# Optimization experiments

Measured on AMD Instinct MI355X. Metric: run time of the kernel, lower is better.

## Reference

```python
import jax, jax.numpy as jnp
import numpy as np

ALPHA = 0.1        # axis_aligned_projection threshold
NEG_INF = -1e30    # large negative used for masking (softmax-equivalent to -inf)


def axis_aligned_projection(x, alpha=ALPHA):
    x_abs = jnp.abs(x)
    max_vals = jnp.max(x_abs, axis=-1, keepdims=True)
    axis_weights = jnp.where(x_abs >= alpha * max_vals, x_abs, 0.0)
    return axis_weights * jnp.sign(x)


def setup_inputs() -> dict:
    key = jax.random.key(0)
    kq, kk, kv = jax.random.split(key, 3)
    B, L, H, E = 4, 2048, 8, 64
    S, D = L, E
    queries = jax.random.normal(kq, (B, L, H, E), dtype=jnp.float32)
    keys = jax.random.normal(kk, (B, S, H, E), dtype=jnp.float32)
    values = jax.random.normal(kv, (B, S, H, D), dtype=jnp.float32)
    # TriangularCausalMask: True strictly above the diagonal -> masked out
    causal = jnp.triu(jnp.ones((L, S), dtype=jnp.bool_), k=1)
    attn_mask = jnp.broadcast_to(causal[None, None], (B, 1, L, S))
    return {"queries": queries, "keys": keys, "values": values, "attn_mask": attn_mask}


def reference(queries, keys, values, attn_mask):
    B, L, H, E = queries.shape
    scale = 1.0 / jnp.sqrt(jnp.float32(E))
    q = axis_aligned_projection(queries)
    k = axis_aligned_projection(keys)
    # [B,H,L,S] dense scores (the module materializes the full matrix)
    scores = jnp.einsum('blhe,bshe->bhls', q, k)
    scores = jnp.where(attn_mask, NEG_INF, scores)
    A = jax.nn.softmax(scale * scores, axis=-1)  # dropout is identity in eval mode
    V = jnp.einsum('bhls,bshd->blhd', A, values)
    return V
```

## Files before the change

### kernel.cpp

```cpp
#include <hip/hip_runtime.h>
#include <hip/hip_bf16.h>
#include <stdint.h>

#define B_ 4
#define L_ 2048
#define H_ 8
#define E_ 64
#define ALPHA 0.1f
#define LOG2E 1.44269504088896f
#define QSCALE (0.125f * LOG2E)


typedef float f32x4 __attribute__((ext_vector_type(4)));
typedef short bf16x8 __attribute__((ext_vector_type(8)));
typedef short bf16x4 __attribute__((ext_vector_type(4)));
typedef uint32_t u32;
typedef unsigned short u16;
typedef u32 u32x2 __attribute__((ext_vector_type(2)));

__device__ __forceinline__ u16 f2bf(float f) {
    u32 x = __builtin_bit_cast(u32, f);
    u32 r = x + 0x7fffu + ((x >> 16) & 1u);
    return (u16)(r >> 16);
}

__device__ __forceinline__ u32 pk2bf(float a, float b) {
    u32 ua = __builtin_bit_cast(u32, a) + 0x8000u;
    u32 ub = __builtin_bit_cast(u32, b) + 0x8000u;
    return (ua >> 16) | (ub & 0xffff0000u);
}

__device__ __forceinline__ f32x4 mfma16x16x16bf16(bf16x4 a, bf16x4 b, f32x4 c) {
#if __has_builtin(__builtin_amdgcn_mfma_f32_16x16x16bf16_1k)
    return __builtin_amdgcn_mfma_f32_16x16x16bf16_1k(a, b, c, 0, 0, 0);
#elif __has_builtin(__builtin_amdgcn_mfma_f32_16x16x16_bf16)
    return __builtin_amdgcn_mfma_f32_16x16x16_bf16(a, b, c, 0, 0, 0);
#else
    f32x4 d;
    asm volatile("v_mfma_f32_16x16x16_bf16 %0, %1, %2, %3"
                 : "=v"(d) : "v"(a), "v"(b), "v"(c));
    return d;
#endif
}

__device__ __forceinline__ void dma16(const u16* g, u16* l) {
    __builtin_amdgcn_global_load_lds(
        (const __attribute__((address_space(1))) void*)g,
        (__attribute__((address_space(3))) void*)l, 16, 0, 0);
}

__global__ __launch_bounds__(256) void prep_kernel(const float* __restrict__ qin,
                                                   const float* __restrict__ kin,
                                                   const float* __restrict__ vin,
                                                   u16* __restrict__ qp,
                                                   u16* __restrict__ kp,
                                                   u16* __restrict__ vt) {
    __shared__ u16 tile[64][66];
    if (blockIdx.x < 4096) {
        const int RG = (B_ * L_ * H_) / 8;
        int wave = threadIdx.x >> 6, lane = threadIdx.x & 63;
        int g = blockIdx.x * 4 + wave;
        const float* src;
        u16* dst;
        int gr;
        float sc;
        bool isq;
        if (g < RG) { src = qin; dst = qp; gr = g; sc = QSCALE; isq = true; }
        else        { src = kin; dst = kp; gr = g - RG; sc = 1.0f; isq = false; }

        int rig = lane >> 3;
        int j = lane & 7;
        int c = j * 4;
        int row = gr * 8 + rig;

        const float* rp = src + (size_t)row * 64;
        float4 v0 = *(const float4*)(rp + c);
        float4 v1 = *(const float4*)(rp + c + 32);
        float f[8] = {v0.x, v0.y, v0.z, v0.w, v1.x, v1.y, v1.z, v1.w};

        float mx = 0.f;
#pragma unroll
        for (int i = 0; i < 8; ++i) mx = fmaxf(mx, fabsf(f[i]));
#pragma unroll
        for (int m = 1; m < 8; m <<= 1) mx = fmaxf(mx, __shfl_xor(mx, m));
        float thr = ALPHA * mx;

        u16 o[8];
#pragma unroll
        for (int i = 0; i < 8; ++i)
            o[i] = (fabsf(f[i]) >= thr) ? f2bf(f[i] * sc) : (u16)0;

        int b = row >> 14;
        int l = (row >> 3) & (L_ - 1);
        int h = row & 7;
        int e0, e1;
        if (isq) {
            e0 = c;
            e1 = c + 32;
        } else {
            int l7 = l & 7;
            e0 = (((j >> 1) ^ l7) << 3) + ((j & 1) << 2);
            e1 = ((((j >> 1) + 4) ^ l7) << 3) + ((j & 1) << 2);
        }
        u16* orow = dst + ((size_t)(b * H_ + h) * L_ + l) * 64;
        uint2 p0 = {(u32)o[0] | ((u32)o[1] << 16), (u32)o[2] | ((u32)o[3] << 16)};
        uint2 p1 = {(u32)o[4] | ((u32)o[5] << 16), (u32)o[6] | ((u32)o[7] << 16)};
        *(uint2*)(orow + e0) = p0;
        *(uint2*)(orow + e1) = p1;
    } else {
        int bx = blockIdx.x - 4096;
        int bh = bx >> 5, sblk = bx & 31;
        int b = bh >> 3, h = bh & 7;
        int t = threadIdx.x;
        int s0 = sblk * 64;

#pragma unroll
        for (int p = 0; p < 2; ++p) {
            int sl = p * 32 + (t >> 3);
            int c = (t & 7) * 4;
            const float* rp = vin + (((size_t)(b * L_ + s0 + sl)) * H_ + h) * 64;
            float4 a = *(const float4*)(rp + c);
            float4 bb = *(const float4*)(rp + c + 32);
            u32* d0 = (u32*)&tile[sl][c];
            d0[0] = (u32)f2bf(a.x) | ((u32)f2bf(a.y) << 16);
            d0[1] = (u32)f2bf(a.z) | ((u32)f2bf(a.w) << 16);
            u32* d1 = (u32*)&tile[sl][c + 32];
            d1[0] = (u32)f2bf(bb.x) | ((u32)f2bf(bb.y) << 16);
            d1[1] = (u32)f2bf(bb.z) | ((u32)f2bf(bb.w) << 16);
        }
        __syncthreads();
#pragma unroll
        for (int p = 0; p < 2; ++p) {
            int d = p * 32 + (t >> 3);
            int c16 = t & 7;
            int sc2 = c16 * 8;
            u16 o[8];
#pragma unroll
            for (int i = 0; i < 8; ++i) o[i] = tile[sc2 + i][d];
            u32 w0 = (u32)o[0] | ((u32)o[1] << 16);
            u32 w1 = (u32)o[2] | ((u32)o[3] << 16);
            u32 w2 = (u32)o[4] | ((u32)o[5] << 16);
            u32 w3 = (u32)o[6] | ((u32)o[7] << 16);
            uint4 val;
            if (d & 1) { val.x = w2; val.y = w3; val.z = w0; val.w = w1; }
            else       { val.x = w0; val.y = w1; val.z = w2; val.w = w3; }
            int pc = c16 ^ ((d >> 1) & 7);
            *(uint4*)(vt + ((size_t)(bh * 32 + sblk) * 64 + d) * 64 + pc * 8) = val;
        }
    }
}

__global__ __launch_bounds__(256, 4) void flash_kernel(const u16* __restrict__ Qp,
                                                       const u16* __restrict__ Kp,
                                                       const u16* __restrict__ Vt,
                                                       float* __restrict__ out) {
    __shared__ u16 kbuf[2][64 * 64];
    __shared__ u16 vbuf[2][64 * 64];
    int t = threadIdx.x;
    int wave = t >> 6, lane = t & 63;
    int bh = blockIdx.x & 31;
    int r5 = blockIdx.x >> 5;
    int g = r5 & 7, kr = r5 >> 3;
    int qq = (kr == 0) ? (31 - g) : (kr == 1) ? (16 + g) : (kr == 2) ? (15 - g) : g;
    int lo = lane & 15, quad = lane >> 4;
    int lo7 = lo & 7;
    int q0 = qq * 64 + wave * 16;
    int b = bh >> 3, h = bh & 7;

    int kc0 = (quad ^ lo7) << 3;
    int kc1 = ((quad + 4) ^ lo7) << 3;

    u32x2 onespk = {0x3F803F80u, 0x3F803F80u};
    bf16x4 vONES = __builtin_bit_cast(bf16x4, onespk);

    const u16* kg0 = Kp + (size_t)bh * L_ * 64 + wave * 512 + lane * 8;
    const u16* vg0 = Vt + (size_t)bh * 32 * 64 * 64 + wave * 512 + lane * 8;

    auto stage = [&](int kt, int buf) {
        const u16* kg = kg0 + (size_t)kt * 4096;
        const u16* vg = vg0 + (size_t)kt * 4096;
        u16* kl = kbuf[buf] + wave * 512;
        u16* vl = vbuf[buf] + wave * 512;
        dma16(kg, kl);
        dma16(kg + 2048, kl + 2048);
        dma16(vg, vl);
        dma16(vg + 2048, vl + 2048);
    };

    const u16* qbase = Qp + ((size_t)bh * L_ + q0 + lo) * 64 + quad * 8;
    bf16x8 aQ0 = *(const bf16x8*)(qbase);
    bf16x8 aQ1 = *(const bf16x8*)(qbase + 32);
    asm volatile("" :: "v"(aQ0), "v"(aQ1));

    f32x4 o[4];
#pragma unroll
    for (int ni = 0; ni < 4; ++ni) o[ni] = (f32x4){0.f, 0.f, 0.f, 0.f};
    f32x4 oL = (f32x4){0.f, 0.f, 0.f, 0.f};

    auto tile_proc = [&](const u16* ks, const u16* vs) {
        bf16x8 k0[4], k1[4];
#pragma unroll
        for (int sub = 0; sub < 4; ++sub) {
            const u16* krow = ks + ((sub * 16 + lo) << 6);
            k0[sub] = *(const bf16x8*)(krow + kc0);
            k1[sub] = *(const bf16x8*)(krow + kc1);
        }
        bf16x4 vf[4][4];
#pragma unroll
        for (int sub = 0; sub < 4; ++sub) {
            int vsw = ((sub * 4 + quad) ^ lo) << 2;
#pragma unroll
            for (int ni = 0; ni < 4; ++ni)
                vf[sub][ni] = *(const bf16x4*)(vs + ((ni * 16 + lo) << 6) + vsw);
        }
        f32x4 S[4];
#pragma unroll
        for (int sub = 0; sub < 4; ++sub) {
            f32x4 acc = {0.f, 0.f, 0.f, 0.f};
            acc = __builtin_amdgcn_mfma_f32_16x16x32_bf16(k0[sub], aQ0, acc, 0, 0, 0);
            S[sub] = __builtin_amdgcn_mfma_f32_16x16x32_bf16(k1[sub], aQ1, acc, 0, 0, 0);
        }
        bf16x4 aP[4];
#pragma unroll
        for (int sub = 0; sub < 4; ++sub) {
            float P0 = __builtin_amdgcn_exp2f(S[sub][0]);
            float P1 = __builtin_amdgcn_exp2f(S[sub][1]);
            float P2 = __builtin_amdgcn_exp2f(S[sub][2]);
            float P3 = __builtin_amdgcn_exp2f(S[sub][3]);
            u32x2 pk = {pk2bf(P0, P1), pk2bf(P2, P3)};
            aP[sub] = __builtin_bit_cast(bf16x4, pk);
        }
#pragma unroll
        for (int sub = 0; sub < 4; ++sub) {
#pragma unroll
            for (int ni = 0; ni < 4; ++ni)
                o[ni] = mfma16x16x16bf16(aP[sub], vf[sub][ni], o[ni]);
            oL = mfma16x16x16bf16(aP[sub], vONES, oL);
        }
    };

    auto frag_proc = [&](const u16* ks, const u16* vs, int sub, bool diag) {
        const u16* krow = ks + ((sub * 16 + lo) << 6);
        bf16x8 k0 = *(const bf16x8*)(krow + kc0);
        bf16x8 k1 = *(const bf16x8*)(krow + kc1);
        f32x4 S = {0.f, 0.f, 0.f, 0.f};
        S = __builtin_amdgcn_mfma_f32_16x16x32_bf16(k0, aQ0, S, 0, 0, 0);
        S = __builtin_amdgcn_mfma_f32_16x16x32_bf16(k1, aQ1, S, 0, 0, 0);

        int vsw = ((sub * 4 + quad) ^ lo) << 2;
        bf16x4 vf[4];
#pragma unroll
        for (int ni = 0; ni < 4; ++ni)
            vf[ni] = *(const bf16x4*)(vs + ((ni * 16 + lo) << 6) + vsw);

        float P[4];
#pragma unroll
        for (int r = 0; r < 4; ++r) {
            float e = __builtin_amdgcn_exp2f(S[r]);
            P[r] = (diag && (quad * 4 + r > lo)) ? 0.f : e;
        }
        u32x2 pk = {pk2bf(P[0], P[1]), pk2bf(P[2], P[3])};
        bf16x4 aP = __builtin_bit_cast(bf16x4, pk);
#pragma unroll
        for (int ni = 0; ni < 4; ++ni)
            o[ni] = mfma16x16x16bf16(aP, vf[ni], o[ni]);
        oL = mfma16x16x16bf16(aP, vONES, oL);
    };

    stage(0, 0);
    __syncthreads();

    for (int kt = 0; kt < qq; ++kt) {
        int cur = kt & 1;
        stage(kt + 1, cur ^ 1);
        tile_proc(kbuf[cur], vbuf[cur]);
        __syncthreads();
    }

    {
        int cur = qq & 1;
        const u16* ks = kbuf[cur];
        const u16* vs = vbuf[cur];
        for (int sub = 0; sub < wave; ++sub) frag_proc(ks, vs, sub, false);
        frag_proc(ks, vs, wave, true);
    }

#pragma unroll
    for (int r = 0; r < 4; ++r) {
        float inv = 1.0f / oL[r];
        int q = q0 + quad * 4 + r;
        float* ob = out + (((size_t)(b * L_ + q)) * H_ + h) * 64 + lo;
        ob[0]  = o[0][r] * inv;
        ob[16] = o[1][r] * inv;
        ob[32] = o[2][r] * inv;
        ob[48] = o[3][r] * inv;
    }
}

extern "C" void kernel_launch(void* const* d_in, const int* in_sizes, int n_in,
                              void* d_out, int out_size, void* d_ws, size_t ws_size,
                              hipStream_t stream) {
    const float* q = (const float*)d_in[0];
    const float* k = (const float*)d_in[1];
    const float* v = (const float*)d_in[2];
    float* out = (float*)d_out;

    const size_t QSZ = (size_t)B_ * H_ * L_ * 64;
    u16* qp = (u16*)d_ws;
    u16* kp = qp + QSZ;
    u16* vt = kp + QSZ;

    prep_kernel<<<5120, 256, 0, stream>>>(q, k, v, qp, kp, vt);
    flash_kernel<<<1024, 256, 0, stream>>>(qp, kp, vt, out);
}
```

Measured before the change: 162.9 us.

## Compute softmax row sums with VALU adds and deepen K/V prefetch pipeline

Replaces the extra MFMA against a ones vector for the softmax denominator with per-lane FP32 adds of the exponentials, followed by a cross-lane shuffle reduction at the end. It also changes the double-buffered load loop to prefetch two tiles ahead, using explicit vmcnt waits and raw barriers instead of __syncthreads. This is meant to cut one MFMA per sub-tile and overlap global-to-LDS DMA more fully with compute. The row sum is now taken from FP32 values rather than the bf16-rounded P, which changes numerics slightly, and the hand-placed waitcnt counts must match the number of outstanding DMAs.

After: 158.0 us, median of 2. -3.0%, faster.

```diff
diff --git a/kernel.cpp b/kernel.cpp
--- a/kernel.cpp
+++ b/kernel.cpp
@@ -170,9 +170,6 @@
     int kc0 = (quad ^ lo7) << 3;
     int kc1 = ((quad + 4) ^ lo7) << 3;
 
-    u32x2 onespk = {0x3F803F80u, 0x3F803F80u};
-    bf16x4 vONES = __builtin_bit_cast(bf16x4, onespk);
-
     const u16* kg0 = Kp + (size_t)bh * L_ * 64 + wave * 512 + lane * 8;
     const u16* vg0 = Vt + (size_t)bh * 32 * 64 * 64 + wave * 512 + lane * 8;
 
@@ -195,7 +192,7 @@
     f32x4 o[4];
 #pragma unroll
     for (int ni = 0; ni < 4; ++ni) o[ni] = (f32x4){0.f, 0.f, 0.f, 0.f};
-    f32x4 oL = (f32x4){0.f, 0.f, 0.f, 0.f};
+    float ls = 0.f;
 
     auto tile_proc = [&](const u16* ks, const u16* vs) {
         bf16x8 k0[4], k1[4];
@@ -227,16 +224,15 @@
             float P1 = __builtin_amdgcn_exp2f(S[sub][1]);
             float P2 = __builtin_amdgcn_exp2f(S[sub][2]);
             float P3 = __builtin_amdgcn_exp2f(S[sub][3]);
+            ls += (P0 + P1) + (P2 + P3);
             u32x2 pk = {pk2bf(P0, P1), pk2bf(P2, P3)};
             aP[sub] = __builtin_bit_cast(bf16x4, pk);
         }
 #pragma unroll
-        for (int sub = 0; sub < 4; ++sub) {
+        for (int sub = 0; sub < 4; ++sub)
 #pragma unroll
             for (int ni = 0; ni < 4; ++ni)
                 o[ni] = mfma16x16x16bf16(aP[sub], vf[sub][ni], o[ni]);
-            oL = mfma16x16x16bf16(aP[sub], vONES, oL);
-        }
     };
 
     auto frag_proc = [&](const u16* ks, const u16* vs, int sub, bool diag) {
@@ -259,35 +255,40 @@
             float e = __builtin_amdgcn_exp2f(S[r]);
             P[r] = (diag && (quad * 4 + r > lo)) ? 0.f : e;
         }
+        ls += (P[0] + P[1]) + (P[2] + P[3]);
         u32x2 pk = {pk2bf(P[0], P[1]), pk2bf(P[2], P[3])};
         bf16x4 aP = __builtin_bit_cast(bf16x4, pk);
 #pragma unroll
         for (int ni = 0; ni < 4; ++ni)
             o[ni] = mfma16x16x16bf16(aP, vf[ni], o[ni]);
-        oL = mfma16x16x16bf16(aP, vONES, oL);
     };
 
     stage(0, 0);
-    __syncthreads();
+    if (qq >= 1) stage(1, 1);
 
     for (int kt = 0; kt < qq; ++kt) {
-        int cur = kt & 1;
-        stage(kt + 1, cur ^ 1);
-        tile_proc(kbuf[cur], vbuf[cur]);
-        __syncthreads();
+        asm volatile("s_waitcnt vmcnt(4)" ::: "memory");
+        __builtin_amdgcn_s_barrier();
+        tile_proc(kbuf[kt & 1], vbuf[kt & 1]);
+        __builtin_amdgcn_s_barrier();
+        if (kt + 2 <= qq) stage(kt + 2, kt & 1);
     }
 
     {
-        int cur = qq & 1;
-        const u16* ks = kbuf[cur];
-        const u16* vs = vbuf[cur];
+        asm volatile("s_waitcnt vmcnt(0)" ::: "memory");
+        __builtin_amdgcn_s_barrier();
+        const u16* ks = kbuf[qq & 1];
+        const u16* vs = vbuf[qq & 1];
         for (int sub = 0; sub < wave; ++sub) frag_proc(ks, vs, sub, false);
         frag_proc(ks, vs, wave, true);
     }
 
+    ls += __shfl_xor(ls, 16);
+    ls += __shfl_xor(ls, 32);
 #pragma unroll
     for (int r = 0; r < 4; ++r) {
-        float inv = 1.0f / oL[r];
+        float lr = __shfl(ls, quad * 4 + r);
+        float inv = 1.0f / lr;
         int q = q0 + quad * 4 + r;
         float* ob = out + (((size_t)(b * L_ + q)) * H_ + h) * 64 + lo;
         ob[0]  = o[0][r] * inv;
```
